# Kernel optimization log

Measured on AMD Instinct MI355X. Metric: run time of the kernel, lower is better.

The kernel has to match this reference:

```python
import jax, jax.numpy as jnp
import numpy as np

B, S, HID = 2, 2048, 2048
NH, NKV, D = 32, 8, 64
M = 256          # FAVOR+ random features
CHUNK = 128      # causal chunk size
EPS = 1e-6


def setup_inputs():
    key = jax.random.key(0)
    ks = jax.random.split(key, 7)
    hidden_states = jax.random.normal(ks[0], (B, S, HID), jnp.float32)
    # RoPE tables (HF Llama style): [B, S, D]
    inv_freq = 1.0 / (10000.0 ** (jnp.arange(0, D, 2, dtype=jnp.float32) / D))
    freqs = jnp.arange(S, dtype=jnp.float32)[:, None] * inv_freq[None, :]   # [S, D/2]
    emb = jnp.concatenate([freqs, freqs], axis=-1)                          # [S, D]
    cos = jnp.broadcast_to(jnp.cos(emb)[None], (B, S, D)).astype(jnp.float32)
    sin = jnp.broadcast_to(jnp.sin(emb)[None], (B, S, D)).astype(jnp.float32)
    sc = 0.02
    Wq = jax.random.normal(ks[1], (NH * D, HID), jnp.float32) * sc
    Wk = jax.random.normal(ks[2], (NKV * D, HID), jnp.float32) * sc
    Wv = jax.random.normal(ks[3], (NKV * D, HID), jnp.float32) * sc
    Wo = jax.random.normal(ks[4], (HID, NH * D), jnp.float32) * sc
    proj = jax.random.normal(ks[5], (M, D), jnp.float32)  # FAVOR+ random projection
    return {"hidden_states": hidden_states, "cos": cos, "sin": sin,
            "Wq": Wq, "Wk": Wk, "Wv": Wv, "Wo": Wo, "proj": proj}


def rotate_half(x):
    x1, x2 = x[..., : x.shape[-1] // 2], x[..., x.shape[-1] // 2:]
    return jnp.concatenate([-x2, x1], axis=-1)


def favor_features(x, proj, is_query):
    # FAVOR+ positive softmax-kernel features: phi(x) = exp(Wx' - |x'|^2/2 - stab)/sqrt(m)
    dn = x.shape[-1] ** -0.25
    xn = x * dn                                            # data normalizer d^{-1/4}
    xp = jnp.einsum('bhsd,md->bhsm', xn, proj)             # [B,H,S,M]
    sq = 0.5 * jnp.sum(xn * xn, axis=-1, keepdims=True)
    if is_query:
        stab = jnp.max(xp, axis=-1, keepdims=True)
    else:
        stab = jnp.max(xp, axis=(-1, -2), keepdims=True)
    return (jnp.exp(xp - sq - stab) + EPS) / jnp.sqrt(jnp.asarray(M, xp.dtype))


def causal_linear_attention(phi_q, phi_k, v):
    # phi_q/phi_k: [B,H,S,M], v: [B,H,S,D]; causal chunked prefix formulation
    Bh, H, T, m = phi_q.shape
    d = v.shape[-1]
    nc = T // CHUNK
    qc = phi_q.reshape(Bh, H, nc, CHUNK, m)
    kc = phi_k.reshape(Bh, H, nc, CHUNK, m)
    vc = v.reshape(Bh, H, nc, CHUNK, d)
    # per-chunk KV state and key sums
    kv = jnp.einsum('bhscm,bhscd->bhsmd', kc, vc)          # [B,H,nc,M,D]
    kz = jnp.sum(kc, axis=3)                               # [B,H,nc,M]
    kv_pre = jnp.cumsum(kv, axis=2) - kv                   # exclusive prefix
    kz_pre = jnp.cumsum(kz, axis=2) - kz
    inter = jnp.einsum('bhscm,bhsmd->bhscd', qc, kv_pre)
    inter_z = jnp.einsum('bhscm,bhsm->bhsc', qc, kz_pre)
    # intra-chunk causal part
    mask = jnp.tril(jnp.ones((CHUNK, CHUNK), phi_q.dtype))
    scores = jnp.einsum('bhscm,bhstm->bhsct', qc, kc) * mask
    intra = jnp.einsum('bhsct,bhstd->bhscd', scores, vc)
    intra_z = jnp.sum(scores, axis=-1)
    out = (inter + intra) / (inter_z + intra_z + EPS)[..., None]
    return out.reshape(Bh, H, T, d)


def reference(hidden_states, cos, sin, Wq, Wk, Wv, Wo, proj):
    b, s, _ = hidden_states.shape
    q = (hidden_states @ Wq.T).reshape(b, s, NH, D).transpose(0, 2, 1, 3)   # [B,NH,S,D]
    k = (hidden_states @ Wk.T).reshape(b, s, NKV, D).transpose(0, 2, 1, 3)  # [B,NKV,S,D]
    v = (hidden_states @ Wv.T).reshape(b, s, NKV, D).transpose(0, 2, 1, 3)
    c, si = cos[:, None, :, :], sin[:, None, :, :]
    q = q * c + rotate_half(q) * si
    k = k * c + rotate_half(k) * si
    groups = NH // NKV
    k = jnp.repeat(k, groups, axis=1)
    v = jnp.repeat(v, groups, axis=1)
    phi_q = favor_features(q, proj, is_query=True)
    phi_k = favor_features(k, proj, is_query=False)
    attn = causal_linear_attention(phi_q, phi_k, v)                         # [B,NH,S,D]
    attn = attn.transpose(0, 2, 1, 3).reshape(b, s, NH * D)
    return attn @ Wo.T
```

## Files before the change

kernel.cpp:

```cpp
#include <hip/hip_runtime.h>
#include <hip/hip_bf16.h>

#define SEQ   2048
#define NHEAD 32
#define NKVH  8
#define DH    64
#define MFEAT 256
#define NCH   16
#define EPSF  1e-6f

typedef __hip_bfloat16 bf16;
typedef unsigned short u16;
typedef __attribute__((ext_vector_type(8))) short short8;
typedef __attribute__((ext_vector_type(4))) float f32x4;

__device__ __forceinline__ float b2f(bf16 x){ return __bfloat162float(x); }
__device__ __forceinline__ bf16  f2b(float x){ return __float2bfloat16(x); }
__device__ __forceinline__ u16   f2u(float x){ bf16 h = __float2bfloat16(x); return *reinterpret_cast<u16*>(&h); }

__device__ __forceinline__ bool probe_f32(const unsigned* __restrict__ p){
  return (p[0] & 0xFFFFu) == 0u;
}
__device__ __forceinline__ float loadIn(const void* __restrict__ ptr, size_t idx, bool f32){
  return f32 ? ((const float*)ptr)[idx] : b2f(((const bf16*)ptr)[idx]);
}

__device__ __forceinline__ void cp16(u16* lds, const u16* g){
  __builtin_amdgcn_global_load_lds((const __attribute__((address_space(1))) unsigned*)g,
      (__attribute__((address_space(3))) unsigned*)lds, 16, 0, 0);
}

#define MFMA16(a,b,c) __builtin_amdgcn_mfma_f32_16x16x32_bf16(a,b,c,0,0,0)

__global__ __launch_bounds__(256) void conv_kernel(const void* __restrict__ src,
    u16* __restrict__ dst, const unsigned* __restrict__ probe)
{
  const bool f32in = probe_f32(probe);
  size_t i = ((size_t)blockIdx.x*256 + threadIdx.x)*4;
  #pragma unroll
  for (int j=0;j<4;++j) dst[i+j] = f2u(loadIn(src, i+j, f32in));
}

__global__ __launch_bounds__(256) void gemm_mfma(const u16* __restrict__ A,
    const u16* __restrict__ W, float* __restrict__ oq, float* __restrict__ ok,
    float* __restrict__ ov, void* __restrict__ outAny, int K, int N, int mode,
    const void* __restrict__ cosg, const void* __restrict__ sing,
    const unsigned* __restrict__ probe)
{
  __shared__ __align__(16) u16 sA[3][4096];
  __shared__ __align__(16) u16 sB[3][4096];
  const int tid = threadIdx.x;
  const int lane = tid & 63, wave = tid >> 6;

  const int nbx = gridDim.x;
  const int nwg = nbx * gridDim.y;
  int id = blockIdx.y * nbx + blockIdx.x;
  int sw = id;
  if ((nwg & 7) == 0) sw = (id & 7) * (nwg >> 3) + (id >> 3);
  const int bx = sw % nbx, by = sw / nbx;
  const int c0 = bx*128, r0 = by*128;

  const int wm = wave & 1, wn = wave >> 1;
  f32x4 acc[4][4] = {};

  const int ch0 = wave*64 + lane, ch1 = 256 + wave*64 + lane;
  const u16* gA0 = A + (size_t)(r0 + (ch0>>2))*K + (ch0&3)*8;
  const u16* gA1 = A + (size_t)(r0 + (ch1>>2))*K + (ch1&3)*8;
  const u16* gB0 = W + (size_t)(c0 + (ch0>>2))*K + (ch0&3)*8;
  const u16* gB1 = W + (size_t)(c0 + (ch1>>2))*K + (ch1&3)*8;
  const int oA0 = (wave*64)*8, oA1 = (256 + wave*64)*8;

  const int pAoff = (wm*64 + (lane&15))*32 + (lane>>4)*8;
  const int pBoff = (wn*64 + (lane&15))*32 + (lane>>4)*8;

  const int nk = K >> 5;

  cp16(&sA[0][oA0], gA0);      cp16(&sA[0][oA1], gA1);
  cp16(&sB[0][oA0], gB0);      cp16(&sB[0][oA1], gB1);
  cp16(&sA[1][oA0], gA0 + 32); cp16(&sA[1][oA1], gA1 + 32);
  cp16(&sB[1][oA0], gB0 + 32); cp16(&sB[1][oA1], gB1 + 32);

  int cur = 0;
  for (int t = 0; t < nk; ++t) {
    if (t < nk-1) asm volatile("s_waitcnt vmcnt(4)" ::: "memory");
    else          asm volatile("s_waitcnt vmcnt(0)" ::: "memory");
    __builtin_amdgcn_s_barrier();
    __builtin_amdgcn_sched_barrier(0);

    if (t + 2 < nk) {
      int stb = cur + 2; if (stb >= 3) stb -= 3;
      const int k0 = (t + 2) * 32;
      cp16(&sA[stb][oA0], gA0 + k0); cp16(&sA[stb][oA1], gA1 + k0);
      cp16(&sB[stb][oA0], gB0 + k0); cp16(&sB[stb][oA1], gB1 + k0);
    }

    const u16* pA = &sA[cur][pAoff];
    const u16* pB = &sB[cur][pBoff];
    short8 af[4], bfv[4];
    #pragma unroll
    for (int mt=0;mt<4;++mt) af[mt]  = *(const short8*)(pA + mt*512);
    #pragma unroll
    for (int nt=0;nt<4;++nt) bfv[nt] = *(const short8*)(pB + nt*512);
    #pragma unroll
    for (int mt=0;mt<4;++mt)
      #pragma unroll
      for (int nt=0;nt<4;++nt)
        acc[mt][nt] = MFMA16(af[mt], bfv[nt], acc[mt][nt]);

    cur = (cur == 2) ? 0 : cur + 1;
  }

  const int rbase = r0 + wm*64 + (lane>>4)*4;
  const int cbase = c0 + wn*64 + (lane&15);
  if (mode == 0) {
    const bool f32o = probe_f32(probe);
    #pragma unroll
    for (int mt=0;mt<4;++mt)
      #pragma unroll
      for (int nt=0;nt<4;++nt)
        #pragma unroll
        for (int rg=0;rg<4;++rg){
          int r = rbase + mt*16 + rg, c = cbase + nt*16;
          float v = acc[mt][nt][rg];
          if (f32o) ((float*)outAny)[(size_t)r*N + c] = v;
          else      ((u16*)outAny)[(size_t)r*N + c] = f2u(v);
        }
  } else {
    const bool f32in = probe_f32(probe);
    const float dn = 0.3535533905932738f;
    #pragma unroll
    for (int nt=0;nt<4;++nt){
      int cc = cbase + nt*16;
      float* dst; int H2, cl; bool isv = false;
      if (cc < 2048){ dst = oq; H2 = 32; cl = cc; }
      else if (cc < 2560){ dst = ok; H2 = 8; cl = cc - 2048; }
      else { dst = ov; H2 = 8; cl = cc - 2560; isv = true; }
      int hh = cl>>6, dd = cl&63;
      float sgn = (dd < 32) ? -1.f : 1.f;
      #pragma unroll
      for (int mt=0;mt<4;++mt)
        #pragma unroll
        for (int rg=0;rg<4;++rg){
          int r = rbase + mt*16 + rg;
          int bb = r>>11, s = r&2047;
          float v = acc[mt][nt][rg];
          if (!isv){
            float vp = acc[mt][nt^2][rg];
            size_t ci = ((size_t)bb*SEQ + s)*DH + dd;
            float cv = loadIn(cosg, ci, f32in);
            float sv = loadIn(sing, ci, f32in);
            v = (v*cv + sgn*vp*sv) * dn;
          }
          dst[(((size_t)bb*H2 + hh)*SEQ + s)*DH + dd] = v;
        }
    }
  }
}

__global__ __launch_bounds__(256) void phi_mfma(const float* __restrict__ xn,
    const u16* __restrict__ projb, float* __restrict__ rmaxk,
    const float* __restrict__ stabk, u16* __restrict__ phi, int mode)
{
  __shared__ __align__(16) u16 sA[64*80];
  __shared__ __align__(16) u16 sP[256*80];
  __shared__ float sq[64];
  const int tid = threadIdx.x, lane = tid & 63, wave = tid >> 6;
  const size_t row0 = (size_t)blockIdx.x * 64;

  #pragma unroll
  for (int l = 0; l < 8; ++l){
    int v8 = tid + l*256;
    int off = v8*8; int m = off>>6, d = off&63;
    *(short8*)&sP[m*80 + d] = ((const short8*)projb)[v8];
  }
  {
    int r = tid >> 2, qq = tid & 3;
    const float* src = xn + (row0 + r)*DH + qq*16;
    float s = 0.f;
    u16 tmp[16];
    #pragma unroll
    for (int i=0;i<16;i+=4){
      float4 v4 = *(const float4*)&src[i];
      s += v4.x*v4.x + v4.y*v4.y + v4.z*v4.z + v4.w*v4.w;
      tmp[i] = f2u(v4.x); tmp[i+1] = f2u(v4.y); tmp[i+2] = f2u(v4.z); tmp[i+3] = f2u(v4.w);
    }
    *(short8*)&sA[r*80 + qq*16]     = *(short8*)&tmp[0];
    *(short8*)&sA[r*80 + qq*16 + 8] = *(short8*)&tmp[8];
    s += __shfl_xor(s, 1, 64);
    s += __shfl_xor(s, 2, 64);
    if (qq == 0) sq[r] = 0.5f*s;
  }
  __syncthreads();

  f32x4 acc[16] = {};
  const u16* pA = &sA[(wave*16 + (lane&15))*80 + (lane>>4)*8];
  short8 af0 = *(const short8*)(pA);
  short8 af1 = *(const short8*)(pA + 32);
  #pragma unroll
  for (int nt=0; nt<16; ++nt){
    const u16* pB = &sP[(nt*16 + (lane&15))*80 + (lane>>4)*8];
    short8 b0 = *(const short8*)(pB);
    short8 b1 = *(const short8*)(pB + 32);
    acc[nt] = MFMA16(af0, b0, acc[nt]);
    acc[nt] = MFMA16(af1, b1, acc[nt]);
  }

  float mx[4];
  #pragma unroll
  for (int rg=0; rg<4; ++rg){
    float m = acc[0][rg];
    #pragma unroll
    for (int nt=1; nt<16; ++nt) m = fmaxf(m, acc[nt][rg]);
    m = fmaxf(m, __shfl_xor(m, 1, 64));
    m = fmaxf(m, __shfl_xor(m, 2, 64));
    m = fmaxf(m, __shfl_xor(m, 4, 64));
    m = fmaxf(m, __shfl_xor(m, 8, 64));
    mx[rg] = m;
  }
  const int rloc = wave*16 + (lane>>4)*4;
  if (mode == 1){
    if ((lane & 15) == 0){
      #pragma unroll
      for (int rg=0;rg<4;++rg) rmaxk[row0 + rloc + rg] = mx[rg];
    }
    return;
  }
  float stab[4];
  if (mode == 0){
    #pragma unroll
    for (int rg=0;rg<4;++rg) stab[rg] = mx[rg];
  } else {
    float s = stabk[row0 >> 11];
    #pragma unroll
    for (int rg=0;rg<4;++rg) stab[rg] = s;
  }
  float sqr[4];
  #pragma unroll
  for (int rg=0;rg<4;++rg) sqr[rg] = sq[rloc + rg];
  #pragma unroll
  for (int nt=0;nt<16;++nt){
    #pragma unroll
    for (int rg=0;rg<4;++rg){
      float val = (__expf(fminf(acc[nt][rg] - sqr[rg] - stab[rg], 0.f)) + EPSF) * 0.0625f;
      phi[(row0 + rloc + rg)*MFEAT + nt*16 + (lane&15)] = f2u(val);
    }
  }
}

__global__ void stab_reduce_kernel(const float* __restrict__ rmaxk, float* __restrict__ stabk){
  __shared__ float red[256];
  int bk = blockIdx.x;
  float mx = -1e30f;
  for (int i = threadIdx.x; i < SEQ; i += 256) mx = fmaxf(mx, rmaxk[(size_t)bk*SEQ + i]);
  red[threadIdx.x] = mx; __syncthreads();
  for (int off=128; off>0; off>>=1){
    if ((int)threadIdx.x < off) red[threadIdx.x] = fmaxf(red[threadIdx.x], red[threadIdx.x+off]);
    __syncthreads();
  }
  if (threadIdx.x==0) stabk[bk] = red[0];
}

__global__ __launch_bounds__(256) void kvchunk_kernel(const bf16* __restrict__ phik,
    const float* __restrict__ vbuf, float* __restrict__ kv, float* __restrict__ kz)
{
  int blk = blockIdx.x; int bk = blk >> 4, c = blk & 15;
  const bf16* Kc = phik + ((size_t)bk*SEQ + c*128)*MFEAT;
  const float* Vc = vbuf + ((size_t)bk*SEQ + c*128)*DH;
  __shared__ float sV[128*64];
  for (int l=0;l<32;++l){ int idx = threadIdx.x + l*256; sV[idx] = Vc[idx]; }
  __syncthreads();
  int m = threadIdx.x;
  float acc[64] = {}; float az = 0.f;
  for (int t=0;t<128;++t){
    float ph = b2f(Kc[(size_t)t*MFEAT + m]);
    az += ph;
    const float4* vr = (const float4*)&sV[t*64];
    #pragma unroll
    for (int d4=0; d4<16; ++d4){
      float4 v4 = vr[d4];
      acc[d4*4+0] += ph*v4.x; acc[d4*4+1] += ph*v4.y;
      acc[d4*4+2] += ph*v4.z; acc[d4*4+3] += ph*v4.w;
    }
  }
  float* out = kv + (size_t)blk*MFEAT*DH + (size_t)m*DH;
  #pragma unroll
  for (int d4=0; d4<16; ++d4)
    ((float4*)out)[d4] = make_float4(acc[d4*4],acc[d4*4+1],acc[d4*4+2],acc[d4*4+3]);
  kz[(size_t)blk*MFEAT + m] = az;
}

__global__ void scan_kernel(float* __restrict__ p, int inner, int nc, int total){
  int t = blockIdx.x*256 + threadIdx.x;
  if (t >= total) return;
  int outer = t / inner, rem = t - outer*inner;
  float* base = p + (size_t)outer*nc*inner + rem;
  float run = 0.f;
  for (int c=0;c<nc;++c){
    float v = base[(size_t)c*inner];
    base[(size_t)c*inner] = run;
    run += v;
  }
}

__global__ __launch_bounds__(256) void attn_mfma(
    const u16* __restrict__ phiq, const u16* __restrict__ phik,
    const float* __restrict__ vbuf, const float* __restrict__ kvp,
    const float* __restrict__ kzp, u16* __restrict__ attnout)
{
  __shared__ __align__(16) u16 smem[28288];
  __shared__ float sZ[128];
  const int tid = threadIdx.x, lane = tid & 63, wave = tid >> 6;
  const int blk = blockIdx.x;
  const int c = blk & 15, h = (blk >> 4) & 31, b = blk >> 9;
  const int kvh = h >> 2;
  const u16* Q   = phiq + (((size_t)(b*NHEAD+h)*SEQ) + c*128)*MFEAT;
  const u16* Kc  = phik + (((size_t)(b*NKVH+kvh)*SEQ) + c*128)*MFEAT;
  const float* Vc  = vbuf + (((size_t)(b*NKVH+kvh)*SEQ) + c*128)*DH;
  const float* KVp = kvp + ((size_t)((b*NKVH+kvh)*NCH + c))*MFEAT*DH;
  const float* KZp = kzp + ((size_t)((b*NKVH+kvh)*NCH + c))*MFEAT;

  u16* sQ   = smem;
  u16* sK   = smem + 4096;
  u16* sKVT = smem + 8192;
  u16* sP   = smem;
  u16* sVT  = smem + 17408;

  f32x4 accS[2][8] = {};
  f32x4 accO[2][5] = {};

  const int ch0 = wave*64 + lane, ch1 = 256 + wave*64 + lane;
  const u16* gQ0 = Q  + (ch0>>2)*MFEAT + (ch0&3)*8;
  const u16* gQ1 = Q  + (ch1>>2)*MFEAT + (ch1&3)*8;
  const u16* gK0 = Kc + (ch0>>2)*MFEAT + (ch0&3)*8;
  const u16* gK1 = Kc + (ch1>>2)*MFEAT + (ch1&3)*8;
  u16* lQ0 = &sQ[(wave*64)*8];  u16* lQ1 = &sQ[(256+wave*64)*8];
  u16* lK0 = &sK[(wave*64)*8];  u16* lK1 = &sK[(256+wave*64)*8];

  for (int k0 = 0; k0 < MFEAT; k0 += 32) {
    cp16(lQ0, gQ0 + k0); cp16(lQ1, gQ1 + k0);
    cp16(lK0, gK0 + k0); cp16(lK1, gK1 + k0);
    #pragma unroll
    for (int i=0;i<8;++i){
      int idx = tid + i*256;
      int m = idx >> 6, d = idx & 63;
      sKVT[d*72 + m] = f2u(KVp[(size_t)(k0+m)*DH + d]);
    }
    if (tid < 32) sKVT[64*72 + tid] = f2u(KZp[k0 + tid]);
    __syncthreads();
    short8 af0, af1;
    const u16* pQ = &sQ[(wave*32 + (lane&15))*32 + (lane>>4)*8];
    af0 = *(const short8*)(pQ);
    af1 = *(const short8*)(pQ + 512);
    #pragma unroll
    for (int nt=0;nt<8;++nt){
      short8 bk = *(const short8*)&sK[(nt*16 + (lane&15))*32 + (lane>>4)*8];
      accS[0][nt] = MFMA16(af0, bk, accS[0][nt]);
      accS[1][nt] = MFMA16(af1, bk, accS[1][nt]);
    }
    #pragma unroll
    for (int nt=0;nt<5;++nt){
      short8 bi = *(const short8*)&sKVT[(nt*16 + (lane&15))*72 + (lane>>4)*8];
      accO[0][nt] = MFMA16(af0, bi, accO[0][nt]);
      accO[1][nt] = MFMA16(af1, bi, accO[1][nt]);
    }
    __syncthreads();
  }

  #pragma unroll
  for (int mt=0;mt<2;++mt){
    int rowb = wave*32 + mt*16 + (lane>>4)*4;
    #pragma unroll
    for (int nt=0;nt<8;++nt){
      int col = nt*16 + (lane&15);
      #pragma unroll
      for (int rg=0;rg<4;++rg){
        int row = rowb + rg;
        float v = (col <= row) ? accS[mt][nt][rg] : 0.f;
        sP[row*136 + col] = f2u(v);
      }
    }
  }
  #pragma unroll
  for (int i=0;i<32;++i){
    int idx = tid + i*256;
    int t = idx >> 6, d = idx & 63;
    sVT[d*136 + t] = f2u(Vc[idx]);
  }
  if (tid < 128) sVT[64*136 + tid] = 0x3F80;
  __syncthreads();

  #pragma unroll
  for (int kc=0;kc<4;++kc){
    const u16* pP = &sP[(wave*32 + (lane&15))*136 + kc*32 + (lane>>4)*8];
    short8 pa0 = *(const short8*)(pP);
    short8 pa1 = *(const short8*)(pP + 16*136);
    #pragma unroll
    for (int nt=0;nt<5;++nt){
      short8 bv = *(const short8*)&sVT[(nt*16 + (lane&15))*136 + kc*32 + (lane>>4)*8];
      accO[0][nt] = MFMA16(pa0, bv, accO[0][nt]);
      accO[1][nt] = MFMA16(pa1, bv, accO[1][nt]);
    }
  }

  if ((lane & 15) == 0){
    #pragma unroll
    for (int mt=0;mt<2;++mt){
      int rowb = wave*32 + mt*16 + (lane>>4)*4;
      #pragma unroll
      for (int rg=0;rg<4;++rg) sZ[rowb + rg] = accO[mt][4][rg];
    }
  }
  __syncthreads();
  const int d0 = lane & 15;
  #pragma unroll
  for (int mt=0;mt<2;++mt){
    int rowb = wave*32 + mt*16 + (lane>>4)*4;
    #pragma unroll
    for (int rg=0;rg<4;++rg){
      int row = rowb + rg;
      float inv = 1.0f / (sZ[row] + EPSF);
      int sg = c*128 + row;
      size_t ob = (((size_t)b*SEQ + sg)*NHEAD + h)*DH;
      #pragma unroll
      for (int nt=0;nt<4;++nt)
        attnout[ob + nt*16 + d0] = f2u(accO[mt][nt][rg] * inv);
    }
  }
}

extern "C" void kernel_launch(void* const* d_in, const int* in_sizes, int n_in,
                              void* d_out, int out_size, void* d_ws, size_t ws_size,
                              hipStream_t stream)
{
  const void* hidden = d_in[0];
  const void* cosg   = d_in[1];
  const void* sing   = d_in[2];
  const void* Wq     = d_in[3];
  const void* Wk     = d_in[4];
  const void* Wv     = d_in[5];
  const void* Wo     = d_in[6];
  const void* proj   = d_in[7];
  const unsigned* probe = (const unsigned*)d_in[1];

  float* ws = (float*)d_ws;
  float* xnq   = ws;
  float* kv    = ws;
  float* kz    = ws + 4194304;
  float* rmaxk = ws + 4259840;
  float* stabk = ws + 4292608;
  float* xnk   = ws + 8388608;
  float* vbuf  = ws + 10485760;
  u16*   projb = (u16*) (ws + 12582912);
  bf16*  phiq  = (bf16*)(ws + 12591104);
  bf16*  phik  = (bf16*)(ws + 29368320);
  u16*   hb    = (u16*) (ws + 33562624);
  u16*   attn  = (u16*) (ws + 33562624);
  u16*   wqkv  = (u16*) (ws + 37756928);
  u16*   wob   = (u16*) (ws + 37756928);

  conv_kernel<<<8192, 256, 0, stream>>>(hidden, hb, probe);
  conv_kernel<<<4096, 256, 0, stream>>>(Wq, wqkv,           probe);
  conv_kernel<<<1024, 256, 0, stream>>>(Wk, wqkv + 4194304, probe);
  conv_kernel<<<1024, 256, 0, stream>>>(Wv, wqkv + 5242880, probe);
  conv_kernel<<<16,   256, 0, stream>>>(proj, projb, probe);

  gemm_mfma<<<dim3(24,32), 256, 0, stream>>>(hb, wqkv, xnq, xnk, vbuf, nullptr,
                                             2048, 3072, 1, cosg, sing, probe);
  conv_kernel<<<4096, 256, 0, stream>>>(Wo, wob, probe);

  phi_mfma<<<2048, 256, 0, stream>>>(xnq, projb, nullptr, nullptr, (u16*)phiq, 0);
  phi_mfma<<<512,  256, 0, stream>>>(xnk, projb, rmaxk, nullptr, nullptr, 1);
  stab_reduce_kernel<<<16, 256, 0, stream>>>(rmaxk, stabk);
  phi_mfma<<<512,  256, 0, stream>>>(xnk, projb, nullptr, stabk, (u16*)phik, 2);

  kvchunk_kernel<<<256, 256, 0, stream>>>(phik, vbuf, kv, kz);
  scan_kernel<<<1024, 256, 0, stream>>>(kv, MFEAT*DH, NCH, 16*MFEAT*DH);
  scan_kernel<<<16,   256, 0, stream>>>(kz, MFEAT,    NCH, 16*MFEAT);

  attn_mfma<<<1024, 256, 0, stream>>>((const u16*)phiq, (const u16*)phik,
                                      vbuf, kv, kz, attn);

  gemm_mfma<<<dim3(16,32), 256, 0, stream>>>(attn, wob, nullptr, nullptr, nullptr,
                                             d_out, 2048, 2048, 0, nullptr, nullptr, probe);
}
```

Measured before the change: 496.4 us.

## Enlarge GEMM tile to 256x128 with 8 waves, BK=64 and XOR-swizzled LDS

The projection GEMMs move from a 128x128 tile with 4 waves and K-step 32 to a 256x128 tile with 8 waves and K-step 64. The triple-buffered LDS layout uses an XOR swizzle to avoid bank conflicts, and the MFMA block is wrapped in s_setprio. This aims to raise arithmetic intensity per global load, halve the number of barriers per K, and cut LDS conflicts. In exchange it uses about 144KB of LDS per block and launches fewer workgroups, which limits occupancy and may leave CUs idle for the 384- and 256-block grids.

```diff
diff --git a/kernel.cpp b/kernel.cpp
--- a/kernel.cpp
+++ b/kernel.cpp
@@ -41,14 +41,14 @@
   for (int j=0;j<4;++j) dst[i+j] = f2u(loadIn(src, i+j, f32in));
 }
 
-__global__ __launch_bounds__(256) void gemm_mfma(const u16* __restrict__ A,
+__global__ __launch_bounds__(512) void gemm_mfma(const u16* __restrict__ A,
     const u16* __restrict__ W, float* __restrict__ oq, float* __restrict__ ok,
     float* __restrict__ ov, void* __restrict__ outAny, int K, int N, int mode,
     const void* __restrict__ cosg, const void* __restrict__ sing,
     const unsigned* __restrict__ probe)
 {
-  __shared__ __align__(16) u16 sA[3][4096];
-  __shared__ __align__(16) u16 sB[3][4096];
+  __shared__ __align__(16) u16 sA[3][16384];
+  __shared__ __align__(16) u16 sB[3][8192];
   const int tid = threadIdx.x;
   const int lane = tid & 63, wave = tid >> 6;
 
@@ -58,57 +58,70 @@
   int sw = id;
   if ((nwg & 7) == 0) sw = (id & 7) * (nwg >> 3) + (id >> 3);
   const int bx = sw % nbx, by = sw / nbx;
-  const int c0 = bx*128, r0 = by*128;
-
-  const int wm = wave & 1, wn = wave >> 1;
+  const int c0 = bx*128, r0 = by*256;
+
+  const int wm = wave >> 1, wn = wave & 1;
   f32x4 acc[4][4] = {};
 
-  const int ch0 = wave*64 + lane, ch1 = 256 + wave*64 + lane;
-  const u16* gA0 = A + (size_t)(r0 + (ch0>>2))*K + (ch0&3)*8;
-  const u16* gA1 = A + (size_t)(r0 + (ch1>>2))*K + (ch1&3)*8;
-  const u16* gB0 = W + (size_t)(c0 + (ch0>>2))*K + (ch0&3)*8;
-  const u16* gB1 = W + (size_t)(c0 + (ch1>>2))*K + (ch1&3)*8;
-  const int oA0 = (wave*64)*8, oA1 = (256 + wave*64)*8;
-
-  const int pAoff = (wm*64 + (lane&15))*32 + (lane>>4)*8;
-  const int pBoff = (wn*64 + (lane&15))*32 + (lane>>4)*8;
-
-  const int nk = K >> 5;
-
-  cp16(&sA[0][oA0], gA0);      cp16(&sA[0][oA1], gA1);
-  cp16(&sB[0][oA0], gB0);      cp16(&sB[0][oA1], gB1);
-  cp16(&sA[1][oA0], gA0 + 32); cp16(&sA[1][oA1], gA1 + 32);
-  cp16(&sB[1][oA0], gB0 + 32); cp16(&sB[1][oA1], gB1 + 32);
+  const int rl  = lane >> 3;
+  const int swzE = ((lane & 7) ^ rl) << 3;
+  const u16* gA = A + (size_t)(r0 + wave*8 + rl)*K + swzE;
+  const u16* gB = W + (size_t)(c0 + wave*8 + rl)*K + swzE;
+  const int aDst = wave*512;
+  const int bDst = wave*512;
+
+  const int rowA = (wm*64 + (lane&15))*64;
+  const int rowB = (wn*64 + (lane&15))*64;
+  const int colS = (((lane>>4)*8) ^ ((lane&7)<<3));
+
+  const int nk = K >> 6;
+
+  #define STAGE(buf, t) do { const int k0_ = (t)*64;                      \
+    cp16(&sA[buf][aDst],         gA + k0_);                               \
+    cp16(&sA[buf][aDst + 4096],  gA + (size_t)64*K  + k0_);               \
+    cp16(&sA[buf][aDst + 8192],  gA + (size_t)128*K + k0_);               \
+    cp16(&sA[buf][aDst + 12288], gA + (size_t)192*K + k0_);               \
+    cp16(&sB[buf][bDst],         gB + k0_);                               \
+    cp16(&sB[buf][bDst + 4096],  gB + (size_t)64*K  + k0_); } while(0)
+
+  STAGE(0, 0);
+  STAGE(1, 1);
 
   int cur = 0;
   for (int t = 0; t < nk; ++t) {
-    if (t < nk-1) asm volatile("s_waitcnt vmcnt(4)" ::: "memory");
+    if (t < nk-1) asm volatile("s_waitcnt vmcnt(6)" ::: "memory");
     else          asm volatile("s_waitcnt vmcnt(0)" ::: "memory");
     __builtin_amdgcn_s_barrier();
     __builtin_amdgcn_sched_barrier(0);
 
-    if (t + 2 < nk) {
-      int stb = cur + 2; if (stb >= 3) stb -= 3;
-      const int k0 = (t + 2) * 32;
-      cp16(&sA[stb][oA0], gA0 + k0); cp16(&sA[stb][oA1], gA1 + k0);
-      cp16(&sB[stb][oA0], gB0 + k0); cp16(&sB[stb][oA1], gB1 + k0);
-    }
-
-    const u16* pA = &sA[cur][pAoff];
-    const u16* pB = &sB[cur][pBoff];
-    short8 af[4], bfv[4];
-    #pragma unroll
-    for (int mt=0;mt<4;++mt) af[mt]  = *(const short8*)(pA + mt*512);
-    #pragma unroll
-    for (int nt=0;nt<4;++nt) bfv[nt] = *(const short8*)(pB + nt*512);
+    if (t + 2 < nk) { int sb = cur + 2; if (sb >= 3) sb -= 3; STAGE(sb, t+2); }
+
+    const u16* bA_ = sA[cur];
+    const u16* bB_ = sB[cur];
+    short8 af[4][2], bfv[4][2];
+    #pragma unroll
+    for (int mt=0;mt<4;++mt){
+      af[mt][0] = *(const short8*)(bA_ + rowA + mt*1024 + colS);
+      af[mt][1] = *(const short8*)(bA_ + rowA + mt*1024 + (colS^32));
+    }
+    #pragma unroll
+    for (int nt=0;nt<4;++nt){
+      bfv[nt][0] = *(const short8*)(bB_ + rowB + nt*1024 + colS);
+      bfv[nt][1] = *(const short8*)(bB_ + rowB + nt*1024 + (colS^32));
+    }
+    __builtin_amdgcn_s_setprio(1);
     #pragma unroll
     for (int mt=0;mt<4;++mt)
       #pragma unroll
-      for (int nt=0;nt<4;++nt)
-        acc[mt][nt] = MFMA16(af[mt], bfv[nt], acc[mt][nt]);
+      for (int nt=0;nt<4;++nt){
+        acc[mt][nt] = MFMA16(af[mt][0], bfv[nt][0], acc[mt][nt]);
+        acc[mt][nt] = MFMA16(af[mt][1], bfv[nt][1], acc[mt][nt]);
+      }
+    __builtin_amdgcn_s_setprio(0);
 
     cur = (cur == 2) ? 0 : cur + 1;
   }
+  #undef STAGE
 
   const int rbase = r0 + wm*64 + (lane>>4)*4;
   const int cbase = c0 + wn*64 + (lane&15);
@@ -464,7 +477,7 @@
   conv_kernel<<<1024, 256, 0, stream>>>(Wv, wqkv + 5242880, probe);
   conv_kernel<<<16,   256, 0, stream>>>(proj, projb, probe);
 
-  gemm_mfma<<<dim3(24,32), 256, 0, stream>>>(hb, wqkv, xnq, xnk, vbuf, nullptr,
+  gemm_mfma<<<dim3(24,16), 512, 0, stream>>>(hb, wqkv, xnq, xnk, vbuf, nullptr,
                                              2048, 3072, 1, cosg, sing, probe);
   conv_kernel<<<4096, 256, 0, stream>>>(Wo, wob, probe);
 
@@ -480,6 +493,6 @@
   attn_mfma<<<1024, 256, 0, stream>>>((const u16*)phiq, (const u16*)phik,
                                       vbuf, kv, kz, attn);
 
-  gemm_mfma<<<dim3(16,32), 256, 0, stream>>>(attn, wob, nullptr, nullptr, nullptr,
+  gemm_mfma<<<dim3(16,16), 512, 0, stream>>>(attn, wob, nullptr, nullptr, nullptr,
                                              d_out, 2048, 2048, 0, nullptr, nullptr, probe);
 }
```

Result: faster. 476.4 us (-4.0%).
